# Kernel optimization log

Measured on AMD Instinct MI355X. Metric: run time of the kernel, lower is better.

The kernel has to match this reference:

```python
import jax, jax.numpy as jnp
import numpy as np

B = 8192; L = 50; D_EMB = 128
N_USER = 100000; N_MOVIE = 50000; N_DENSE = 8
D = 2 * D_EMB + D_EMB + N_DENSE  # 392 total_input_dim
E = 4; T = 2; H1 = 256; H2 = 128; ATT_H = 64; N_CROSS = 3


def setup_inputs() -> dict:
    key = jax.random.key(0)
    ks = jax.random.split(key, 28)
    rn = lambda k, shape, s=0.02: jax.random.normal(k, shape, jnp.float32) * s
    inp = {
        'userId': jax.random.randint(ks[0], (B,), 0, N_USER),
        'movieId': jax.random.randint(ks[1], (B,), 0, N_MOVIE),
        'seq_history': jax.random.randint(ks[2], (B, L), 0, N_MOVIE),
        'dense_feats': jax.random.normal(ks[3], (B, N_DENSE), jnp.float32),
        # embeddings (row 0 is padding_idx -> zeros)
        'emb_user': rn(ks[4], (N_USER + 1, D_EMB)).at[0].set(0.0),
        'emb_movie': rn(ks[5], (N_MOVIE + 1, D_EMB)).at[0].set(0.0),
        # DIN attention MLP: input [q,k,q-k,q*k] = 4*D_EMB
        'att_w1': rn(ks[6], (4 * D_EMB, ATT_H)), 'att_b1': jnp.zeros((ATT_H,), jnp.float32),
        'att_w2': rn(ks[7], (ATT_H, 1)), 'att_b2': jnp.zeros((1,), jnp.float32),
        # LayerNorms
        'in_gamma': jnp.ones((D,), jnp.float32), 'in_beta': jnp.zeros((D,), jnp.float32),
        'cr_gamma': jnp.ones((D,), jnp.float32), 'cr_beta': jnp.zeros((D,), jnp.float32),
        # CrossNetV2: x_{l+1} = x0 * (x_l W_l + b_l) + x_l
        'cross_W': rn(ks[8], (N_CROSS, D, D)), 'cross_b': jnp.zeros((N_CROSS, D), jnp.float32),
        # MMoE experts: Linear(D,H1)-ReLU-Linear(H1,H2), batched over E
        'exp_w1': rn(ks[9], (E, D, H1)), 'exp_b1': jnp.zeros((E, H1), jnp.float32),
        'exp_w2': rn(ks[10], (E, H1, H2)), 'exp_b2': jnp.zeros((E, H2), jnp.float32),
        # gates per task
        'gate_w': rn(ks[11], (T, D, E)), 'gate_b': jnp.zeros((T, E), jnp.float32),
        # task heads Linear(H2, 1)
        'head_w': rn(ks[12], (T, H2)), 'head_b': jnp.zeros((T,), jnp.float32),
    }
    return inp


def _layernorm(x, g, b, eps=1e-5):
    m = jnp.mean(x, axis=-1, keepdims=True)
    v = jnp.var(x, axis=-1, keepdims=True)
    return (x - m) * jax.lax.rsqrt(v + eps) * g + b


def _forward(userId, movieId, seq_history, dense_feats, emb_user, emb_movie,
             att_w1, att_b1, att_w2, att_b2, in_gamma, in_beta,
             cross_W, cross_b, cr_gamma, cr_beta,
             exp_w1, exp_b1, exp_w2, exp_b2, gate_w, gate_b, head_w, head_b):
    # sparse embedding gathers
    user_e = emb_user[userId]            # [B, D_EMB]
    movie_e = emb_movie[movieId]         # [B, D_EMB]  (target item)
    hist = emb_movie[seq_history]        # [B, L, D_EMB]
    mask = seq_history > 0               # [B, L]

    # DIN attention pooling
    q = jnp.broadcast_to(movie_e[:, None, :], hist.shape)            # [B, L, D_EMB]
    att_in = jnp.concatenate([q, hist, q - hist, q * hist], axis=-1)  # [B, L, 4*D_EMB]
    scores = (jax.nn.relu(att_in @ att_w1 + att_b1) @ att_w2 + att_b2)[..., 0]  # [B, L]
    scores = jnp.where(mask, scores, -1e9)
    probs = jax.nn.softmax(scores, axis=-1)                           # [B, L]
    interest = jnp.einsum('bl,bld->bd', probs, hist)                  # [B, D_EMB]

    x = jnp.concatenate([user_e, movie_e, interest, dense_feats], axis=-1)  # [B, D]
    x = _layernorm(x, in_gamma, in_beta)

    # CrossNetV2
    x0 = x
    for l in range(N_CROSS):
        x = x0 * (x @ cross_W[l] + cross_b[l]) + x
    x = _layernorm(x, cr_gamma, cr_beta)

    # MMoE: batched expert GEMMs + per-task soft gates
    h = jax.nn.relu(jnp.einsum('bd,edh->ebh', x, exp_w1) + exp_b1[:, None, :])  # [E,B,H1]
    eo = jnp.einsum('ebh,eho->ebo', h, exp_w2) + exp_b2[:, None, :]             # [E,B,H2]
    g = jax.nn.softmax(jnp.einsum('bd,tde->tbe', x, gate_w) + gate_b[:, None, :], axis=-1)  # [T,B,E]
    task_feat = jnp.einsum('tbe,ebo->tbo', g, eo)                                # [T,B,H2]

    logits = jnp.einsum('tbo,to->tb', task_feat, head_w) + head_b[:, None]       # [T,B]
    return logits


def reference(userId, movieId, seq_history, dense_feats, emb_user, emb_movie,
              att_w1, att_b1, att_w2, att_b2, in_gamma, in_beta,
              cross_W, cross_b, cr_gamma, cr_beta,
              exp_w1, exp_b1, exp_w2, exp_b2, gate_w, gate_b, head_w, head_b):
    return _forward(userId, movieId, seq_history, dense_feats, emb_user, emb_movie,
                    att_w1, att_b1, att_w2, att_b2, in_gamma, in_beta,
                    cross_W, cross_b, cr_gamma, cr_beta,
                    exp_w1, exp_b1, exp_w2, exp_b2, gate_w, gate_b, head_w, head_b)
```

## Files before the change

kernel.cpp:

```cpp
#include <hip/hip_runtime.h>
#include <hip/hip_bf16.h>

typedef short short8 __attribute__((ext_vector_type(8)));
typedef short short4v __attribute__((ext_vector_type(4)));
typedef float f32x4 __attribute__((ext_vector_type(4)));

constexpr int BB = 8192;
constexpr int LL = 50;
constexpr int DE = 128;
constexpr int DD = 392;
constexpr int HH1 = 256;
constexpr int HH2 = 128;

__device__ __forceinline__ short f2b(float x) {
    __hip_bfloat16 h = __float2bfloat16(x);
    return __builtin_bit_cast(short, h);
}
__device__ __forceinline__ float b2f(short v) {
    unsigned u = ((unsigned)(unsigned short)v) << 16;
    return __builtin_bit_cast(float, u);
}

__global__ __launch_bounds__(256) void prep_small(
    const float* __restrict__ w1,
    const float* __restrict__ w2, const float* __restrict__ b2,
    const float* __restrict__ head_w,
    short* __restrict__ WqpT, short* __restrict__ WkpF,
    float* __restrict__ hw2, float* __restrict__ hc)
{
    __shared__ float hw[256];
    const int b = blockIdx.x, t = threadIdx.x;
    if (b < 32) {
        int o = b * 256 + t;
        int h = o >> 7, d = o & 127;
        WqpT[o] = f2b(w1[d * 64 + h] + w1[16384 + d * 64 + h]);
    } else if (b < 64) {
        int o = (b - 32) * 256 + t;
        int e = o & 7, lane = (o >> 3) & 63, nt = (o >> 9) & 3, kt = o >> 11;
        int k = (kt << 5) + ((lane >> 4) << 3) + e;
        int h = (nt << 4) + (lane & 15);
        int base = (o >> 3) << 4;
        WkpF[base + e]     = f2b(w1[(128 + k) * 64 + h] - w1[(256 + k) * 64 + h]);
        WkpF[base + 8 + e] = f2b(w1[(384 + k) * 64 + h]);
    } else {
        const int e = b - 64;
        hw[t] = head_w[t];
        __syncthreads();
        const float* row = &w2[((long)e * HH1 + t) * HH2];
        float s0 = 0.f, s1 = 0.f;
        #pragma unroll 8
        for (int o = 0; o < 128; o += 4) {
            float4 v = *reinterpret_cast<const float4*>(&row[o]);
            s0 += v.x * hw[o] + v.y * hw[o + 1] + v.z * hw[o + 2] + v.w * hw[o + 3];
            s1 += v.x * hw[128 + o] + v.y * hw[129 + o] + v.z * hw[130 + o] + v.w * hw[131 + o];
        }
        hw2[(((e << 8) + t) << 1) + 0] = s0;
        hw2[(((e << 8) + t) << 1) + 1] = s1;
        if (t < 2) {
            float s = 0.f;
            for (int o = 0; o < 128; ++o) s += b2[e * 128 + o] * hw[t * 128 + o];
            hc[e * 2 + t] = s;
        }
    }
}

constexpr int S0 = 3 * 392 * 392;
constexpr int S1 = 4 * 392 * 256;
constexpr int S2 = (50001 * 128) / 4;

__global__ __launch_bounds__(256) void prep_trans(
    const float* __restrict__ cross_W, const float* __restrict__ exp_w1,
    const float* __restrict__ emb_movie,
    short* __restrict__ WTc, short* __restrict__ WT1, short* __restrict__ embB)
{
    int idx = blockIdx.x * 256 + threadIdx.x;
    if (idx < S0) {
        int z = idx / (392 * 392), rr = idx - z * 392 * 392;
        int c = rr / 392, r = rr - c * 392;
        WTc[idx] = f2b(cross_W[(long)z * 153664 + r * 392 + c]);
    } else if (idx < S0 + S1) {
        int j = idx - S0;
        int z = j / 100352, rr = j - z * 100352;
        int c = rr / 392, r = rr - c * 392;
        WT1[j] = f2b(exp_w1[(long)z * 100352 + r * 256 + c]);
    } else if (idx < S0 + S1 + S2) {
        long j = (long)(idx - S0 - S1) << 2;
        float4 v = *reinterpret_cast<const float4*>(&emb_movie[j]);
        short4v o;
        o[0] = f2b(v.x); o[1] = f2b(v.y); o[2] = f2b(v.z); o[3] = f2b(v.w);
        *reinterpret_cast<short4v*>(&embB[j]) = o;
    }
}

__global__ __launch_bounds__(256, 8) void attn_kernel(
    const int* __restrict__ userId, const int* __restrict__ movieId,
    const int* __restrict__ seq, const float* __restrict__ dense,
    const float* __restrict__ emb_user, const float* __restrict__ emb_movie,
    const short* __restrict__ embB,
    const short* __restrict__ WqpT, const short* __restrict__ WkpF,
    const float* __restrict__ att_b1, const float* __restrict__ att_w2,
    const float* __restrict__ att_b2,
    const float* __restrict__ in_gamma, const float* __restrict__ in_beta,
    float* __restrict__ x0f, short* __restrict__ x0b)
{
    __shared__ short hist[64 * 128];
    __shared__ float qs[128];
    __shared__ int   seq_s[64];
    __shared__ float sp[4][64];
    __shared__ float spS[4][64];
    __shared__ float probs[64];
    __shared__ float ibuf[4][128];
    __shared__ float stats[2];

    const int b = blockIdx.x;
    const int t = threadIdx.x;
    const int lane = t & 63;
    const int w = t >> 6;

    if (t < 128) qs[t] = emb_movie[(long)movieId[b] * DE + t];
    if (t < 64)  seq_s[t] = (t < LL) ? seq[b * LL + t] : 0;
    __syncthreads();

    #pragma unroll
    for (int i = 0; i < 4; ++i) {
        const int idx = t + (i << 8);
        const int l = idx >> 4, c = idx & 15;
        short8 hv = *reinterpret_cast<const short8*>(&embB[(long)seq_s[l] * DE + (c << 3)]);
        const int byte = (l << 8) + ((c << 4) ^ ((l & 7) << 4));
        *reinterpret_cast<short8*>(reinterpret_cast<char*>(hist) + byte) = hv;
    }

    float ue = (t < 128) ? emb_user[(long)userId[b] * DE + t] : 0.f;
    float dv = (t >= 128 && t < 136) ? dense[b * 8 + (t - 128)] : 0.f;

    short8 bfrag[4];
    #pragma unroll
    for (int kt = 0; kt < 4; ++kt) {
        const int fo = ((((kt << 2) + w) << 6) | lane) << 4;
        short8 wk = *reinterpret_cast<const short8*>(&WkpF[fo]);
        short8 wp = *reinterpret_cast<const short8*>(&WkpF[fo + 8]);
        const int kq = (kt << 5) + ((lane >> 4) << 3);
        #pragma unroll
        for (int j = 0; j < 8; ++j)
            bfrag[kt][j] = f2b(fmaf(qs[kq + j], b2f(wp[j]), b2f(wk[j])));
    }

    {
        float s = 0.f;
        const short* wq = &WqpT[(lane << 7) + (w << 5)];
        #pragma unroll
        for (int c = 0; c < 4; ++c) {
            short8 wv = *reinterpret_cast<const short8*>(&wq[c << 3]);
            #pragma unroll
            for (int j = 0; j < 8; ++j)
                s = fmaf(qs[(w << 5) + (c << 3) + j], b2f(wv[j]), s);
        }
        sp[w][lane] = s;
    }
    __syncthreads();

    {
        const int col = (w << 4) + (lane & 15);
        const float qc = att_b1[col] + sp[0][col] + sp[1][col] + sp[2][col] + sp[3][col];
        const float w2v = att_w2[col];
        #pragma unroll
        for (int mt = 0; mt < 4; ++mt) {
            f32x4 acc = {0.f, 0.f, 0.f, 0.f};
            const int row = (mt << 4) + (lane & 15);
            const int rbase = row << 8;
            const int swz = (row & 7) << 4;
            #pragma unroll
            for (int kt = 0; kt < 4; ++kt) {
                const int kbyte = (kt << 6) + ((lane >> 4) << 4);
                short8 a = *reinterpret_cast<const short8*>(
                    reinterpret_cast<char*>(hist) + rbase + (kbyte ^ swz));
                acc = __builtin_amdgcn_mfma_f32_16x16x32_bf16(a, bfrag[kt], acc, 0, 0, 0);
            }
            #pragma unroll
            for (int r = 0; r < 4; ++r) {
                float v = fmaxf(acc[r] + qc, 0.f) * w2v;
                v += __shfl_xor(v, 1); v += __shfl_xor(v, 2);
                v += __shfl_xor(v, 4); v += __shfl_xor(v, 8);
                if ((lane & 15) == 0)
                    spS[w][(mt << 4) + ((lane >> 4) << 2) + r] = v;
            }
        }
    }
    __syncthreads();

    if (t < 64) {
        float sc = spS[0][t] + spS[1][t] + spS[2][t] + spS[3][t] + att_b2[0];
        float s = (t < LL) ? ((seq_s[t] > 0) ? sc : -1e9f) : -INFINITY;
        float m = s;
        #pragma unroll
        for (int off = 32; off > 0; off >>= 1) m = fmaxf(m, __shfl_xor(m, off));
        float e = (t < LL) ? __expf(s - m) : 0.f;
        float sum = e;
        #pragma unroll
        for (int off = 32; off > 0; off >>= 1) sum += __shfl_xor(sum, off);
        probs[t] = (t < LL) ? (e / sum) : 0.f;
    }
    __syncthreads();

    const int g  = t >> 5;
    const int d0 = (t & 31) << 2;
    float4 ps = make_float4(0.f, 0.f, 0.f, 0.f);
    #pragma unroll
    for (int i = 0; i < 8; ++i) {
        const int l = g + (i << 3);
        const int byte = (l << 8) + ((d0 << 1) ^ ((l & 7) << 4));
        short4v hv = *reinterpret_cast<const short4v*>(
            reinterpret_cast<const char*>(hist) + byte);
        const float p = probs[l];
        ps.x = fmaf(p, b2f(hv[0]), ps.x);
        ps.y = fmaf(p, b2f(hv[1]), ps.y);
        ps.z = fmaf(p, b2f(hv[2]), ps.z);
        ps.w = fmaf(p, b2f(hv[3]), ps.w);
    }
    ps.x += __shfl_xor(ps.x, 32); ps.y += __shfl_xor(ps.y, 32);
    ps.z += __shfl_xor(ps.z, 32); ps.w += __shfl_xor(ps.w, 32);
    if (lane < 32)
        *reinterpret_cast<float4*>(&ibuf[w][lane << 2]) = ps;
    __syncthreads();

    float v0 = (t < 128) ? ue : qs[t - 128];
    float v1 = 0.f;
    if (t < 128)       v1 = ibuf[0][t] + ibuf[1][t] + ibuf[2][t] + ibuf[3][t];
    else if (t < 136)  v1 = dv;

    float s2 = v0 + v1, q2 = v0 * v0 + v1 * v1;
    #pragma unroll
    for (int off = 32; off > 0; off >>= 1) {
        s2 += __shfl_xor(s2, off);
        q2 += __shfl_xor(q2, off);
    }
    if (lane == 0) { sp[0][w] = s2; sp[1][w] = q2; }
    __syncthreads();
    if (t == 0) {
        float S = sp[0][0] + sp[0][1] + sp[0][2] + sp[0][3];
        float Q = sp[1][0] + sp[1][1] + sp[1][2] + sp[1][3];
        float mean = S / (float)DD;
        float var = Q / (float)DD - mean * mean;
        stats[0] = mean;
        stats[1] = rsqrtf(var + 1e-5f);
    }
    __syncthreads();
    const float mean = stats[0], inv = stats[1];
    const long base = (long)b * DD;
    float o0 = (v0 - mean) * inv * in_gamma[t] + in_beta[t];
    x0f[base + t] = o0; x0b[base + t] = f2b(o0);
    if (t < 136) {
        float o1 = (v1 - mean) * inv * in_gamma[256 + t] + in_beta[256 + t];
        x0f[base + 256 + t] = o1; x0b[base + 256 + t] = f2b(o1);
    }
}

template<int MODE, int WF32, int WB16, int NXB, int NZB>
__global__ __launch_bounds__(256) void bgemm(
    const short* __restrict__ A, const short* __restrict__ WT,
    const float* __restrict__ bias,
    float* __restrict__ outF, short* __restrict__ outB,
    const float* __restrict__ x0, const float* __restrict__ xin,
    int M, int N, int K, long aZ, long wZ, long bZ, long oZ)
{
    __shared__ short As[2][64 * 64];
    __shared__ short Bs[2][64 * 64];

    int id = blockIdx.x;
    const int qq = (int)gridDim.x >> 3;
    id = (id & 7) * qq + (id >> 3);
    const int mb  = id / (NXB * NZB);
    const int rem = id - mb * (NXB * NZB);
    const int z   = rem / NXB;
    const int xb  = rem - z * NXB;

    A += (long)z * aZ; WT += (long)z * wZ; bias += (long)z * bZ;
    const long oz = (long)z * oZ;

    const int t = threadIdx.x, w = t >> 6, lane = t & 63;
    const int m0 = mb * 64, n0 = xb * 64;
    const int sm = t >> 3, sk8 = (t & 7) << 3;

    f32x4 acc[4];
    #pragma unroll
    for (int i = 0; i < 4; ++i) {
        #pragma unroll
        for (int r = 0; r < 4; ++r) acc[i][r] = 0.f;
    }

    const int nsteps = (K + 63) >> 6;
    short8 avA[2], bvA[2], avB[2], bvB[2];

    auto loadA = [&](int k0) {
        #pragma unroll
        for (int i = 0; i < 2; ++i) {
            const int r = sm + (i << 5);
            short8 zv = {0, 0, 0, 0, 0, 0, 0, 0};
            avA[i] = zv; bvA[i] = zv;
            if (k0 + sk8 < K) {
                avA[i] = *reinterpret_cast<const short8*>(&A[(long)(m0 + r) * K + k0 + sk8]);
                if (n0 + r < N)
                    bvA[i] = *reinterpret_cast<const short8*>(&WT[(long)(n0 + r) * K + k0 + sk8]);
            }
        }
    };
    auto loadB = [&](int k0) {
        #pragma unroll
        for (int i = 0; i < 2; ++i) {
            const int r = sm + (i << 5);
            short8 zv = {0, 0, 0, 0, 0, 0, 0, 0};
            avB[i] = zv; bvB[i] = zv;
            if (k0 + sk8 < K) {
                avB[i] = *reinterpret_cast<const short8*>(&A[(long)(m0 + r) * K + k0 + sk8]);
                if (n0 + r < N)
                    bvB[i] = *reinterpret_cast<const short8*>(&WT[(long)(n0 + r) * K + k0 + sk8]);
            }
        }
    };
    auto wrA = [&](int buf) {
        #pragma unroll
        for (int i = 0; i < 2; ++i) {
            const int r = sm + (i << 5);
            const int byte = (r << 7) + ((sk8 << 1) ^ ((r & 7) << 4));
            *reinterpret_cast<short8*>(reinterpret_cast<char*>(&As[buf][0]) + byte) = avA[i];
            *reinterpret_cast<short8*>(reinterpret_cast<char*>(&Bs[buf][0]) + byte) = bvA[i];
        }
    };
    auto wrB = [&](int buf) {
        #pragma unroll
        for (int i = 0; i < 2; ++i) {
            const int r = sm + (i << 5);
            const int byte = (r << 7) + ((sk8 << 1) ^ ((r & 7) << 4));
            *reinterpret_cast<short8*>(reinterpret_cast<char*>(&As[buf][0]) + byte) = avB[i];
            *reinterpret_cast<short8*>(reinterpret_cast<char*>(&Bs[buf][0]) + byte) = bvB[i];
        }
    };
    auto domfma = [&](int buf) {
        #pragma unroll
        for (int kt = 0; kt < 2; ++kt) {
            const int kbyte = (kt << 6) + ((lane >> 4) << 4);
            const int ar = (w << 4) + (lane & 15);
            short8 a = *reinterpret_cast<const short8*>(
                reinterpret_cast<char*>(&As[buf][0]) + (ar << 7) + (kbyte ^ ((ar & 7) << 4)));
            #pragma unroll
            for (int nt = 0; nt < 4; ++nt) {
                const int br = (nt << 4) + (lane & 15);
                short8 bb = *reinterpret_cast<const short8*>(
                    reinterpret_cast<char*>(&Bs[buf][0]) + (br << 7) + (kbyte ^ ((br & 7) << 4)));
                acc[nt] = __builtin_amdgcn_mfma_f32_16x16x32_bf16(a, bb, acc[nt], 0, 0, 0);
            }
        }
    };

    loadA(0);
    wrA(0);
    if (nsteps > 1) loadA(64);
    if (nsteps > 2) loadB(128);
    __syncthreads();

    int cur = 0, s = 0;
    while (s + 1 < nsteps) {
        domfma(cur);
        wrA(cur ^ 1);
        if (s + 3 < nsteps) loadA((s + 3) << 6);
        __syncthreads(); cur ^= 1; ++s;
        if (s + 1 < nsteps) {
            domfma(cur);
            wrB(cur ^ 1);
            if (s + 3 < nsteps) loadB((s + 3) << 6);
            __syncthreads(); cur ^= 1; ++s;
        }
    }
    domfma(cur);

    #pragma unroll
    for (int nt = 0; nt < 4; ++nt) {
        const int col = n0 + (nt << 4) + (lane & 15);
        if (col < N) {
            const float bv = bias[col];
            #pragma unroll
            for (int r = 0; r < 4; ++r) {
                const int row = m0 + (w << 4) + ((lane >> 4) << 2) + r;
                float v = acc[nt][r] + bv;
                if (MODE == 1) v = fmaxf(v, 0.f);
                const long o = (long)row * N + col;
                if (MODE == 2) v = x0[o] * v + xin[o];
                if (WF32) outF[oz + o] = v;
                if (WB16) outB[oz + o] = f2b(v);
            }
        }
    }
}

__global__ __launch_bounds__(256) void ln_kernel(
    const float* __restrict__ in,
    const float* __restrict__ gamma, const float* __restrict__ beta,
    float* __restrict__ outF, short* __restrict__ outB)
{
    __shared__ float red[2][4];
    __shared__ float stats[2];
    const int b = blockIdx.x, t = threadIdx.x, lane = t & 63, w = t >> 6;
    const long base = (long)b * DD;
    float v0 = in[base + t];
    float v1 = (t < 136) ? in[base + 256 + t] : 0.f;
    float s = v0 + v1, q2 = v0 * v0 + v1 * v1;
    #pragma unroll
    for (int off = 32; off > 0; off >>= 1) {
        s += __shfl_xor(s, off);
        q2 += __shfl_xor(q2, off);
    }
    if (lane == 0) { red[0][w] = s; red[1][w] = q2; }
    __syncthreads();
    if (t == 0) {
        float S = red[0][0] + red[0][1] + red[0][2] + red[0][3];
        float Q = red[1][0] + red[1][1] + red[1][2] + red[1][3];
        float mean = S / (float)DD;
        float var = Q / (float)DD - mean * mean;
        stats[0] = mean;
        stats[1] = rsqrtf(var + 1e-5f);
    }
    __syncthreads();
    const float mean = stats[0], inv = stats[1];
    float o0 = (v0 - mean) * inv * gamma[t] + beta[t];
    outF[base + t] = o0; outB[base + t] = f2b(o0);
    if (t < 136) {
        float o1 = (v1 - mean) * inv * gamma[256 + t] + beta[256 + t];
        outF[base + 256 + t] = o1; outB[base + 256 + t] = f2b(o1);
    }
}

__global__ __launch_bounds__(256) void final_kernel(
    const float* __restrict__ x, const short* __restrict__ h1,
    const float* __restrict__ hw2, const float* __restrict__ hc,
    const float* __restrict__ gate_w, const float* __restrict__ gate_b,
    const float* __restrict__ head_b, float* __restrict__ out)
{
    const int t = threadIdx.x, lane = t & 63, w = t >> 6;
    const int b = blockIdx.x * 4 + w;
    const float* xr = x + (long)b * DD;

    float xv[7];
    #pragma unroll
    for (int i = 0; i < 7; ++i) {
        int d = lane + (i << 6);
        xv[i] = (d < DD) ? xr[d] : 0.f;
    }

    float gl[8] = {0.f, 0.f, 0.f, 0.f, 0.f, 0.f, 0.f, 0.f};
    #pragma unroll
    for (int i = 0; i < 7; ++i) {
        int d = lane + (i << 6);
        if (d < DD) {
            float4 g0 = *reinterpret_cast<const float4*>(&gate_w[d << 2]);
            float4 g1 = *reinterpret_cast<const float4*>(&gate_w[1568 + (d << 2)]);
            gl[0] = fmaf(xv[i], g0.x, gl[0]); gl[1] = fmaf(xv[i], g0.y, gl[1]);
            gl[2] = fmaf(xv[i], g0.z, gl[2]); gl[3] = fmaf(xv[i], g0.w, gl[3]);
            gl[4] = fmaf(xv[i], g1.x, gl[4]); gl[5] = fmaf(xv[i], g1.y, gl[5]);
            gl[6] = fmaf(xv[i], g1.z, gl[6]); gl[7] = fmaf(xv[i], g1.w, gl[7]);
        }
    }

    float ed[8];
    #pragma unroll
    for (int e = 0; e < 4; ++e) {
        short4v hv = *reinterpret_cast<const short4v*>(
            &h1[((long)e * BB + b) * HH1 + (lane << 2)]);
        const float* hwp = &hw2[(((e << 8) + (lane << 2))) << 1];
        float4 w01 = *reinterpret_cast<const float4*>(hwp);
        float4 w23 = *reinterpret_cast<const float4*>(hwp + 4);
        float h0 = b2f(hv[0]), h1f = b2f(hv[1]), h2 = b2f(hv[2]), h3 = b2f(hv[3]);
        ed[e]     = fmaf(h0, w01.x, fmaf(h1f, w01.z, fmaf(h2, w23.x, h3 * w23.z)));
        ed[4 + e] = fmaf(h0, w01.y, fmaf(h1f, w01.w, fmaf(h2, w23.y, h3 * w23.w)));
    }

    #pragma unroll
    for (int v = 0; v < 8; ++v) {
        #pragma unroll
        for (int off = 32; off > 0; off >>= 1) {
            gl[v] += __shfl_xor(gl[v], off);
            ed[v] += __shfl_xor(ed[v], off);
        }
    }

    if (lane == 0) {
        float res[2];
        #pragma unroll
        for (int tt = 0; tt < 2; ++tt) {
            float lv[4], m = -1e30f;
            #pragma unroll
            for (int e = 0; e < 4; ++e) {
                lv[e] = gl[tt * 4 + e] + gate_b[tt * 4 + e];
                m = fmaxf(m, lv[e]);
            }
            float sum = 0.f, acc = 0.f;
            #pragma unroll
            for (int e = 0; e < 4; ++e) { lv[e] = __expf(lv[e] - m); sum += lv[e]; }
            #pragma unroll
            for (int e = 0; e < 4; ++e)
                acc = fmaf(lv[e], ed[tt * 4 + e] + hc[e * 2 + tt], acc);
            res[tt] = head_b[tt] + acc / sum;
        }
        out[b] = res[0];
        out[BB + b] = res[1];
    }
}

extern "C" void kernel_launch(void* const* d_in, const int* in_sizes, int n_in,
                              void* d_out, int out_size, void* d_ws, size_t ws_size,
                              hipStream_t stream) {
    const int*   userId    = (const int*)d_in[0];
    const int*   movieId   = (const int*)d_in[1];
    const int*   seq       = (const int*)d_in[2];
    const float* dense     = (const float*)d_in[3];
    const float* emb_user  = (const float*)d_in[4];
    const float* emb_movie = (const float*)d_in[5];
    const float* att_w1    = (const float*)d_in[6];
    const float* att_b1    = (const float*)d_in[7];
    const float* att_w2    = (const float*)d_in[8];
    const float* att_b2    = (const float*)d_in[9];
    const float* in_gamma  = (const float*)d_in[10];
    const float* in_beta   = (const float*)d_in[11];
    const float* cr_gamma  = (const float*)d_in[12];
    const float* cr_beta   = (const float*)d_in[13];
    const float* cross_W   = (const float*)d_in[14];
    const float* cross_b   = (const float*)d_in[15];
    const float* exp_w1    = (const float*)d_in[16];
    const float* exp_b1    = (const float*)d_in[17];
    const float* exp_w2    = (const float*)d_in[18];
    const float* exp_b2    = (const float*)d_in[19];
    const float* gate_w    = (const float*)d_in[20];
    const float* gate_b    = (const float*)d_in[21];
    const float* head_w    = (const float*)d_in[22];
    const float* head_b    = (const float*)d_in[23];
    float* outp = (float*)d_out;

    char* p = (char*)d_ws;
    auto alloc = [&](size_t bytes) -> char* {
        char* r = p; p += (bytes + 255) & ~(size_t)255; return r;
    };
    short* WqpT = (short*)alloc(8192 * 2);
    short* WkpF = (short*)alloc(16384 * 2);
    float* hw2 = (float*)alloc(2048 * 4);
    float* hc  = (float*)alloc(8 * 4);
    short* WTc = (short*)alloc((size_t)3 * 392 * 392 * 2);
    short* WT1 = (short*)alloc((size_t)4 * 256 * 392 * 2);
    short* embB = (short*)alloc((size_t)50001 * 128 * 2);
    float* x0f = (float*)alloc((size_t)BB * DD * 4);
    short* x0b = (short*)alloc((size_t)BB * DD * 2);
    float* xAf = (float*)alloc((size_t)BB * DD * 4);
    short* xAb = (short*)alloc((size_t)BB * DD * 2);
    float* xBf = (float*)alloc((size_t)BB * DD * 4);
    short* xBb = (short*)alloc((size_t)BB * DD * 2);
    short* h1b = (short*)alloc((size_t)4 * BB * HH1 * 2);

    prep_small<<<68, 256, 0, stream>>>(att_w1, exp_w2, exp_b2, head_w,
                                       WqpT, WkpF, hw2, hc);
    prep_trans<<<(S0 + S1 + S2 + 255) / 256, 256, 0, stream>>>(
        cross_W, exp_w1, emb_movie, WTc, WT1, embB);

    attn_kernel<<<BB, 256, 0, stream>>>(userId, movieId, seq, dense,
                                        emb_user, emb_movie, embB,
                                        WqpT, WkpF,
                                        att_b1, att_w2, att_b2,
                                        in_gamma, in_beta, x0f, x0b);

    bgemm<2, 1, 1, 7, 1><<<896, 256, 0, stream>>>(x0b, WTc, cross_b, xAf, xAb,
                                                  x0f, x0f, BB, DD, DD, 0, 0, 0, 0);
    bgemm<2, 1, 1, 7, 1><<<896, 256, 0, stream>>>(xAb, WTc + 392 * 392, cross_b + 392,
                                                  xBf, xBb, x0f, xAf, BB, DD, DD, 0, 0, 0, 0);
    bgemm<2, 1, 0, 7, 1><<<896, 256, 0, stream>>>(xBb, WTc + 2 * 392 * 392, cross_b + 784,
                                                  xAf, nullptr, x0f, xBf, BB, DD, DD, 0, 0, 0, 0);

    ln_kernel<<<BB, 256, 0, stream>>>(xAf, cr_gamma, cr_beta, xBf, xBb);

    bgemm<1, 0, 1, 4, 4><<<2048, 256, 0, stream>>>(
        xBb, WT1, exp_b1, nullptr, h1b, nullptr, nullptr,
        BB, HH1, DD, 0, (long)HH1 * DD, HH1, (long)BB * HH1);

    final_kernel<<<BB / 4, 256, 0, stream>>>(xBf, h1b, hw2, hc,
                                             gate_w, gate_b, head_b, outp);

    (void)in_sizes; (void)n_in; (void)out_size; (void)ws_size;
}
```

Baseline: 174.3 us.

## Precompute per-sample query projection with a batched GEMM before attention

Moves the per-row query projection (q·(Wq+Wq-k) plus bias) out of the attention kernel into a separate bf16 GEMM over all 8192 query embeddings, gathered and converted to bf16 in the prep kernel. The attention kernel then reads one precomputed value per column and drops a reduction stage and a barrier. The key-side weights are also kept in fp32, so the B-fragment is built without an intermediate bf16 rounding. This adds a kernel launch plus extra global traffic for qb and qcAll, and the query projection now runs on bf16 inputs.

```diff
diff --git a/kernel.cpp b/kernel.cpp
--- a/kernel.cpp
+++ b/kernel.cpp
@@ -25,7 +25,7 @@
     const float* __restrict__ w1,
     const float* __restrict__ w2, const float* __restrict__ b2,
     const float* __restrict__ head_w,
-    short* __restrict__ WqpT, short* __restrict__ WkpF,
+    short* __restrict__ WqpT, float* __restrict__ WkpFf,
     float* __restrict__ hw2, float* __restrict__ hc)
 {
     __shared__ float hw[256];
@@ -40,8 +40,8 @@
         int k = (kt << 5) + ((lane >> 4) << 3) + e;
         int h = (nt << 4) + (lane & 15);
         int base = (o >> 3) << 4;
-        WkpF[base + e]     = f2b(w1[(128 + k) * 64 + h] - w1[(256 + k) * 64 + h]);
-        WkpF[base + 8 + e] = f2b(w1[(384 + k) * 64 + h]);
+        WkpFf[base + e]     = w1[(128 + k) * 64 + h] - w1[(256 + k) * 64 + h];
+        WkpFf[base + 8 + e] = w1[(384 + k) * 64 + h];
     } else {
         const int e = b - 64;
         hw[t] = head_w[t];
@@ -67,11 +67,13 @@
 constexpr int S0 = 3 * 392 * 392;
 constexpr int S1 = 4 * 392 * 256;
 constexpr int S2 = (50001 * 128) / 4;
+constexpr int S3 = (BB * 128) / 4;
 
 __global__ __launch_bounds__(256) void prep_trans(
     const float* __restrict__ cross_W, const float* __restrict__ exp_w1,
-    const float* __restrict__ emb_movie,
-    short* __restrict__ WTc, short* __restrict__ WT1, short* __restrict__ embB)
+    const float* __restrict__ emb_movie, const int* __restrict__ movieId,
+    short* __restrict__ WTc, short* __restrict__ WT1, short* __restrict__ embB,
+    short* __restrict__ qb)
 {
     int idx = blockIdx.x * 256 + threadIdx.x;
     if (idx < S0) {
@@ -89,6 +91,14 @@
         short4v o;
         o[0] = f2b(v.x); o[1] = f2b(v.y); o[2] = f2b(v.z); o[3] = f2b(v.w);
         *reinterpret_cast<short4v*>(&embB[j]) = o;
+    } else if (idx < S0 + S1 + S2 + S3) {
+        int j = idx - S0 - S1 - S2;
+        int bb = j >> 5, d0 = (j & 31) << 2;
+        float4 v = *reinterpret_cast<const float4*>(
+            &emb_movie[(long)movieId[bb] * DE + d0]);
+        short4v o;
+        o[0] = f2b(v.x); o[1] = f2b(v.y); o[2] = f2b(v.z); o[3] = f2b(v.w);
+        *reinterpret_cast<short4v*>(&qb[bb * DE + d0]) = o;
     }
 }
 
@@ -97,16 +107,14 @@
     const int* __restrict__ seq, const float* __restrict__ dense,
     const float* __restrict__ emb_user, const float* __restrict__ emb_movie,
     const short* __restrict__ embB,
-    const short* __restrict__ WqpT, const short* __restrict__ WkpF,
-    const float* __restrict__ att_b1, const float* __restrict__ att_w2,
-    const float* __restrict__ att_b2,
+    const float* __restrict__ qcAll, const float* __restrict__ WkpFf,
+    const float* __restrict__ att_w2, const float* __restrict__ att_b2,
     const float* __restrict__ in_gamma, const float* __restrict__ in_beta,
     float* __restrict__ x0f, short* __restrict__ x0b)
 {
     __shared__ short hist[64 * 128];
     __shared__ float qs[128];
     __shared__ int   seq_s[64];
-    __shared__ float sp[4][64];
     __shared__ float spS[4][64];
     __shared__ float probs[64];
     __shared__ float ibuf[4][128];
@@ -130,60 +138,43 @@
         *reinterpret_cast<short8*>(reinterpret_cast<char*>(hist) + byte) = hv;
     }
 
+    const int col = (w << 4) + (lane & 15);
     float ue = (t < 128) ? emb_user[(long)userId[b] * DE + t] : 0.f;
     float dv = (t >= 128 && t < 136) ? dense[b * 8 + (t - 128)] : 0.f;
+    const float qc  = qcAll[((long)b << 6) + col];
+    const float w2v = att_w2[col];
 
     short8 bfrag[4];
     #pragma unroll
     for (int kt = 0; kt < 4; ++kt) {
-        const int fo = ((((kt << 2) + w) << 6) | lane) << 4;
-        short8 wk = *reinterpret_cast<const short8*>(&WkpF[fo]);
-        short8 wp = *reinterpret_cast<const short8*>(&WkpF[fo + 8]);
+        const float* wkp = &WkpFf[((((kt << 2) + w) << 6) | lane) << 4];
         const int kq = (kt << 5) + ((lane >> 4) << 3);
         #pragma unroll
         for (int j = 0; j < 8; ++j)
-            bfrag[kt][j] = f2b(fmaf(qs[kq + j], b2f(wp[j]), b2f(wk[j])));
-    }
-
-    {
-        float s = 0.f;
-        const short* wq = &WqpT[(lane << 7) + (w << 5)];
-        #pragma unroll
-        for (int c = 0; c < 4; ++c) {
-            short8 wv = *reinterpret_cast<const short8*>(&wq[c << 3]);
-            #pragma unroll
-            for (int j = 0; j < 8; ++j)
-                s = fmaf(qs[(w << 5) + (c << 3) + j], b2f(wv[j]), s);
-        }
-        sp[w][lane] = s;
-    }
-    __syncthreads();
-
-    {
-        const int col = (w << 4) + (lane & 15);
-        const float qc = att_b1[col] + sp[0][col] + sp[1][col] + sp[2][col] + sp[3][col];
-        const float w2v = att_w2[col];
-        #pragma unroll
-        for (int mt = 0; mt < 4; ++mt) {
-            f32x4 acc = {0.f, 0.f, 0.f, 0.f};
-            const int row = (mt << 4) + (lane & 15);
-            const int rbase = row << 8;
-            const int swz = (row & 7) << 4;
-            #pragma unroll
-            for (int kt = 0; kt < 4; ++kt) {
-                const int kbyte = (kt << 6) + ((lane >> 4) << 4);
-                short8 a = *reinterpret_cast<const short8*>(
-                    reinterpret_cast<char*>(hist) + rbase + (kbyte ^ swz));
-                acc = __builtin_amdgcn_mfma_f32_16x16x32_bf16(a, bfrag[kt], acc, 0, 0, 0);
-            }
-            #pragma unroll
-            for (int r = 0; r < 4; ++r) {
-                float v = fmaxf(acc[r] + qc, 0.f) * w2v;
-                v += __shfl_xor(v, 1); v += __shfl_xor(v, 2);
-                v += __shfl_xor(v, 4); v += __shfl_xor(v, 8);
-                if ((lane & 15) == 0)
-                    spS[w][(mt << 4) + ((lane >> 4) << 2) + r] = v;
-            }
+            bfrag[kt][j] = f2b(fmaf(qs[kq + j], wkp[8 + j], wkp[j]));
+    }
+    __syncthreads();
+
+    #pragma unroll
+    for (int mt = 0; mt < 4; ++mt) {
+        f32x4 acc = {0.f, 0.f, 0.f, 0.f};
+        const int row = (mt << 4) + (lane & 15);
+        const int rbase = row << 8;
+        const int swz = (row & 7) << 4;
+        #pragma unroll
+        for (int kt = 0; kt < 4; ++kt) {
+            const int kbyte = (kt << 6) + ((lane >> 4) << 4);
+            short8 a = *reinterpret_cast<const short8*>(
+                reinterpret_cast<char*>(hist) + rbase + (kbyte ^ swz));
+            acc = __builtin_amdgcn_mfma_f32_16x16x32_bf16(a, bfrag[kt], acc, 0, 0, 0);
+        }
+        #pragma unroll
+        for (int r = 0; r < 4; ++r) {
+            float v = fmaxf(acc[r] + qc, 0.f) * w2v;
+            v += __shfl_xor(v, 1); v += __shfl_xor(v, 2);
+            v += __shfl_xor(v, 4); v += __shfl_xor(v, 8);
+            if ((lane & 15) == 0)
+                spS[w][(mt << 4) + ((lane >> 4) << 2) + r] = v;
         }
     }
     __syncthreads();
@@ -234,11 +225,11 @@
         s2 += __shfl_xor(s2, off);
         q2 += __shfl_xor(q2, off);
     }
-    if (lane == 0) { sp[0][w] = s2; sp[1][w] = q2; }
+    if (lane == 0) { spS[0][w] = s2; spS[1][w] = q2; }
     __syncthreads();
     if (t == 0) {
-        float S = sp[0][0] + sp[0][1] + sp[0][2] + sp[0][3];
-        float Q = sp[1][0] + sp[1][1] + sp[1][2] + sp[1][3];
+        float S = spS[0][0] + spS[0][1] + spS[0][2] + spS[0][3];
+        float Q = spS[1][0] + spS[1][1] + spS[1][2] + spS[1][3];
         float mean = S / (float)DD;
         float var = Q / (float)DD - mean * mean;
         stats[0] = mean;
@@ -538,13 +529,15 @@
     auto alloc = [&](size_t bytes) -> char* {
         char* r = p; p += (bytes + 255) & ~(size_t)255; return r;
     };
-    short* WqpT = (short*)alloc(8192 * 2);
-    short* WkpF = (short*)alloc(16384 * 2);
+    short* WqpT  = (short*)alloc(8192 * 2);
+    float* WkpFf = (float*)alloc(16384 * 4);
     float* hw2 = (float*)alloc(2048 * 4);
     float* hc  = (float*)alloc(8 * 4);
     short* WTc = (short*)alloc((size_t)3 * 392 * 392 * 2);
     short* WT1 = (short*)alloc((size_t)4 * 256 * 392 * 2);
     short* embB = (short*)alloc((size_t)50001 * 128 * 2);
+    short* qb   = (short*)alloc((size_t)BB * DE * 2);
+    float* qcAll = (float*)alloc((size_t)BB * 64 * 4);
     float* x0f = (float*)alloc((size_t)BB * DD * 4);
     short* x0b = (short*)alloc((size_t)BB * DD * 2);
     float* xAf = (float*)alloc((size_t)BB * DD * 4);
@@ -554,14 +547,18 @@
     short* h1b = (short*)alloc((size_t)4 * BB * HH1 * 2);
 
     prep_small<<<68, 256, 0, stream>>>(att_w1, exp_w2, exp_b2, head_w,
-                                       WqpT, WkpF, hw2, hc);
-    prep_trans<<<(S0 + S1 + S2 + 255) / 256, 256, 0, stream>>>(
-        cross_W, exp_w1, emb_movie, WTc, WT1, embB);
+                                       WqpT, WkpFf, hw2, hc);
+    prep_trans<<<(S0 + S1 + S2 + S3 + 255) / 256, 256, 0, stream>>>(
+        cross_W, exp_w1, emb_movie, movieId, WTc, WT1, embB, qb);
+
+    bgemm<0, 1, 0, 1, 1><<<128, 256, 0, stream>>>(
+        qb, WqpT, att_b1, qcAll, nullptr, nullptr, nullptr,
+        BB, 64, DE, 0, 0, 0, 0);
 
     attn_kernel<<<BB, 256, 0, stream>>>(userId, movieId, seq, dense,
                                         emb_user, emb_movie, embB,
-                                        WqpT, WkpF,
-                                        att_b1, att_w2, att_b2,
+                                        qcAll, WkpFf,
+                                        att_w2, att_b2,
                                         in_gamma, in_beta, x0f, x0b);
 
     bgemm<2, 1, 1, 7, 1><<<896, 256, 0, stream>>>(x0b, WTc, cross_b, xAf, xAb,
```

Result: no change. 177.2 us (+1.7%).
